# Kernel tuning notes

Hardware: AMD Instinct MI355X
Metric: run time of the kernel (lower is better)

Reference implementation:

```python
import jax, jax.numpy as jnp
import numpy as np
from jax import lax

B, T, PRED_LEN = 1024, 100, 30
E, H, IN = 512, 1024, 2


def _gru_cell(h, gx, Whh, bhh):
    # PyTorch GRU cell. gx = x @ Wih.T + bih precomputed, shape (B, 3H).
    gh = h @ Whh.T + bhh
    gx_r, gx_z, gx_n = jnp.split(gx, 3, axis=-1)
    gh_r, gh_z, gh_n = jnp.split(gh, 3, axis=-1)
    r = jax.nn.sigmoid(gx_r + gh_r)
    z = jax.nn.sigmoid(gx_z + gh_z)
    n = jnp.tanh(gx_n + r * gh_n)
    return (1.0 - z) * n + z * h


def _run_gru(x, h0, Wih, Whh, bih, bhh):
    # x: (B, T, F) -> outputs (B, T, H), final hidden (B, H)
    gx = jnp.einsum('btf,gf->btg', x, Wih) + bih  # batch all input projections
    def step(h, gxt):
        h_new = _gru_cell(h, gxt, Whh, bhh)
        return h_new, h_new
    h_last, ys = lax.scan(step, h0, jnp.swapaxes(gx, 0, 1))
    return jnp.swapaxes(ys, 0, 1), h_last


def setup_inputs() -> dict:
    key = jax.random.key(0)
    ks = iter(jax.random.split(key, 32))
    s = 1.0 / np.sqrt(H)
    u = lambda k, shp: jax.random.uniform(k, shp, jnp.float32, -s, s)
    inp = {'obs': jax.random.normal(next(ks), (B, T, IN), jnp.float32)}
    inp['We'] = u(next(ks), (E, IN)); inp['be'] = u(next(ks), (E,))
    inp['Wed'] = u(next(ks), (E, 2)); inp['bed'] = u(next(ks), (E,))
    for name, fin in [('enc1', E), ('enc2', H), ('dec1', E), ('dec2', H)]:
        inp[name + '_Wih'] = u(next(ks), (3 * H, fin))
        inp[name + '_Whh'] = u(next(ks), (3 * H, H))
        inp[name + '_bih'] = u(next(ks), (3 * H,))
        inp[name + '_bhh'] = u(next(ks), (3 * H,))
    inp['Wout'] = u(next(ks), (2, H)); inp['bout'] = u(next(ks), (2,))
    return inp


def reference(obs, We, be, Wed, bed,
              enc1_Wih, enc1_Whh, enc1_bih, enc1_bhh,
              enc2_Wih, enc2_Whh, enc2_bih, enc2_bhh,
              dec1_Wih, dec1_Whh, dec1_bih, dec1_bhh,
              dec2_Wih, dec2_Whh, dec2_bih, dec2_bhh,
              Wout, bout):
    b = obs.shape[0]
    h0 = jnp.zeros((b, H), obs.dtype)
    # --- encoder ---
    emb = jnp.tanh(jnp.einsum('bti,ei->bte', obs, We) + be)
    enc1, h = _run_gru(emb, h0, enc1_Wih, enc1_Whh, enc1_bih, enc1_bhh)
    # quirk preserved: hidden from gru1 is fed as h0 of gru2
    enc2, h = _run_gru(enc1, h, enc2_Wih, enc2_Whh, enc2_bih, enc2_bhh)
    out_loc0 = enc2[:, -2, :] @ Wout.T + bout  # second-to-last step (B, 2)
    def dec_step(carry, _):
        hc, last = carry
        d_emb = jnp.tanh(last @ Wed.T + bed)
        h1 = _gru_cell(hc, d_emb @ dec1_Wih.T + dec1_bih, dec1_Whh, dec1_bhh)
        h2 = _gru_cell(h1, h1 @ dec2_Wih.T + dec2_bih, dec2_Whh, dec2_bhh)
        out = h2 @ Wout.T + bout
        return (h2, out), out
    _, preds = lax.scan(dec_step, (h, out_loc0), None, length=PRED_LEN)
    return jnp.swapaxes(preds, 0, 1)  # (B, pred_len, 2)
```

## Files before the change

### kernel.cpp

```cpp
#include <hip/hip_runtime.h>
#include <stdint.h>

#define NB 1024
#define NT 100
#define NPRED 30
#define NE 512
#define NH 1024
#define NG (3*NH)

typedef unsigned short u16;
typedef unsigned int u32;
typedef u16 u16x4 __attribute__((ext_vector_type(4)));
typedef float f32x4 __attribute__((ext_vector_type(4)));
typedef __bf16 bf16x8 __attribute__((ext_vector_type(8)));

__device__ __forceinline__ u16 f2b(float f){
  u32 u = __float_as_uint(f);
  u = (u + 0x7FFFu + ((u >> 16) & 1u)) >> 16;
  return (u16)u;
}
__device__ __forceinline__ float sig_(float x){ return 1.0f/(1.0f+__expf(-x)); }
__device__ __forceinline__ float tanh_(float x){
  float e = __expf(2.0f*fabsf(x));
  return copysignf(1.0f - 2.0f/(e+1.0f), x);
}

__global__ void cvt_kernel(const float* src, u16* dst, int n4){
  int i = blockIdx.x*256 + threadIdx.x;
  if (i < n4){
    f32x4 v = ((const f32x4*)src)[i];
    u16x4 o;
    o[0]=f2b(v[0]); o[1]=f2b(v[1]); o[2]=f2b(v[2]); o[3]=f2b(v[3]);
    ((u16x4*)dst)[i] = o;
  }
}

__global__ void emb_kernel(const float* __restrict__ obs, const float* __restrict__ We,
                           const float* __restrict__ be, u16* __restrict__ out, int t){
  int idx = blockIdx.x*256 + threadIdx.x;
  int b = idx >> 9, e = idx & 511;
  float x0 = obs[(b*NT + t)*2], x1 = obs[(b*NT + t)*2 + 1];
  out[idx] = f2b(tanh_(We[e*2]*x0 + We[e*2+1]*x1 + be[e]));
}

__device__ __forceinline__ void gload16(const u16* g, const u16* lds){
  __builtin_amdgcn_global_load_lds(
      (const __attribute__((address_space(1))) void*)g,
      (__attribute__((address_space(3))) void*)lds, 16, 0, 0);
}

__device__ __forceinline__ void gemm_tile_body(
    const u16* __restrict__ A, int lda,
    const u16* __restrict__ W, int K,
    const float* __restrict__ bias, float* __restrict__ C,
    int bRow, int bCol)
{
  __shared__ __align__(16) u16 As[2][128][64];
  __shared__ __align__(16) u16 Bs[2][128][64];

  const int tid = threadIdx.x;
  const int w = tid >> 6, l = tid & 63;
  const int wm = w >> 1, wn = w & 1;
  const int fr = l & 15, lhi = l >> 4;
  const int srow = l >> 3;
  const int gcol = (((l & 7) ^ srow) * 8);

  f32x4 acc[4][4];
  #pragma unroll
  for (int m=0;m<4;m++)
    #pragma unroll
    for (int n=0;n<4;n++) acc[m][n] = (f32x4)0.0f;

  const u16* Ab = A + (size_t)bRow*lda + gcol;
  const u16* Wb = W + (size_t)bCol*K + gcol;
  const int NK = K >> 6;

  #pragma unroll
  for (int s4=0;s4<4;s4++){
    int slab = w*4 + s4;
    int row = slab*8 + srow;
    gload16(Ab + (size_t)row*lda, &As[0][slab*8][0]);
    gload16(Wb + (size_t)row*K,   &Bs[0][slab*8][0]);
  }
  __syncthreads();

  for (int t = 0; t < NK; ++t){
    const int cur = t & 1;
    if (t + 1 < NK){
      const int k0 = (t+1)*64;
      #pragma unroll
      for (int s4=0;s4<4;s4++){
        int slab = w*4 + s4;
        int row = slab*8 + srow;
        gload16(Ab + (size_t)row*lda + k0, &As[cur^1][slab*8][0]);
        gload16(Wb + (size_t)row*K   + k0, &Bs[cur^1][slab*8][0]);
      }
    }
    const u16* Ac = &As[cur][0][0];
    const u16* Bc = &Bs[cur][0][0];
    #pragma unroll
    for (int kk=0; kk<2; ++kk){
      const int ch = (((kk*4 + lhi) ^ (l & 7)) * 8);
      bf16x8 af[4], bfr[4];
      #pragma unroll
      for (int m=0;m<4;m++)
        af[m] = *(const bf16x8*)(Ac + (size_t)(wm*64 + m*16 + fr)*64 + ch);
      #pragma unroll
      for (int n=0;n<4;n++)
        bfr[n] = *(const bf16x8*)(Bc + (size_t)(wn*64 + n*16 + fr)*64 + ch);
      #pragma unroll
      for (int m=0;m<4;m++)
        #pragma unroll
        for (int n=0;n<4;n++)
          acc[m][n] = __builtin_amdgcn_mfma_f32_16x16x32_bf16(af[m], bfr[n], acc[m][n], 0, 0, 0);
    }
    __syncthreads();
  }

  const int crow = lhi * 4, ccol = l & 15;
  #pragma unroll
  for (int n=0;n<4;n++){
    int col = bCol + wn*64 + n*16 + ccol;
    float bv = bias[col];
    #pragma unroll
    for (int m=0;m<4;m++){
      int row = bRow + wm*64 + m*16 + crow;
      float* Cp = C + (size_t)row*NG + col;
      #pragma unroll
      for (int r=0;r<4;r++)
        __builtin_nontemporal_store(acc[m][n][r] + bv, Cp + (size_t)r*NG);
    }
  }
}

__global__ __launch_bounds__(256)
void gemm_dual_kernel(
  const u16* A0, int lda0, int K0, const u16* W0, const float* bias0, float* C0,
  const u16* A1, int lda1, int K1, const u16* W1, const float* bias1, float* C1)
{
  const int id = blockIdx.x;
  const int xcd = id & 7, k = id >> 3;
  const int cb = 3*xcd + (k >> 4);
  const int rem = k & 15;
  const int rb = rem >> 1;
  const int z  = rem & 1;

  if (z == 0)
    gemm_tile_body(A0, lda0, W0, K0, bias0, C0, rb*128, cb*128);
  else
    gemm_tile_body(A1, lda1, W1, K1, bias1, C1, rb*128, cb*128);
}

__device__ __forceinline__ void cell_core(
    const float* __restrict__ gx, const float* __restrict__ gh,
    const float* __restrict__ hin, float* __restrict__ hout,
    u16* __restrict__ houtb, u16* __restrict__ seq,
    int b, int jq, f32x4& o)
{
  int idx = b*256 + jq;
  int base = b*768;
  const f32x4* gx4 = (const f32x4*)gx;
  const f32x4* gh4 = (const f32x4*)gh;
  f32x4 xr = gx4[base + jq], xz = gx4[base + 256 + jq], xn = gx4[base + 512 + jq];
  f32x4 hr = gh4[base + jq], hz = gh4[base + 256 + jq], hn = gh4[base + 512 + jq];
  f32x4 hv = ((const f32x4*)hin)[idx];
  u16x4 ob;
  #pragma unroll
  for (int c=0;c<4;c++){
    float r = sig_(xr[c] + hr[c]);
    float z = sig_(xz[c] + hz[c]);
    float n = tanh_(xn[c] + r*hn[c]);
    float h = (1.0f - z)*n + z*hv[c];
    o[c] = h; ob[c] = f2b(h);
  }
  ((f32x4*)hout)[idx] = o;
  ((u16x4*)houtb)[idx] = ob;
  if (seq) ((u16x4*)seq)[idx] = ob;
}

__global__ void gru_cell_kernel(const float* __restrict__ gx, const float* __restrict__ gh,
                                const float* __restrict__ hin, float* __restrict__ hout,
                                u16* __restrict__ houtb, u16* __restrict__ seq)
{
  f32x4 o;
  cell_core(gx, gh, hin, hout, houtb, seq, blockIdx.x, threadIdx.x, o);
}

__global__ void gru_cell_emb_kernel(const float* __restrict__ gx, const float* __restrict__ gh,
                                    const float* __restrict__ hin, float* __restrict__ hout,
                                    u16* __restrict__ houtb, u16* __restrict__ seq,
                                    const float* __restrict__ obs, const float* __restrict__ We,
                                    const float* __restrict__ be, u16* __restrict__ embb, int et)
{
  int b = blockIdx.x, tid = threadIdx.x;
  f32x4 o;
  cell_core(gx, gh, hin, hout, houtb, seq, b, tid, o);
  if (embb){
    float x0 = obs[(b*NT + et)*2], x1 = obs[(b*NT + et)*2 + 1];
    int e0 = tid*2;
    u16 v0 = f2b(tanh_(We[e0*2]  *x0 + We[e0*2+1]*x1 + be[e0]));
    u16 v1 = f2b(tanh_(We[e0*2+2]*x0 + We[e0*2+3]*x1 + be[e0+1]));
    ((u32*)embb)[b*256 + tid] = (u32)v0 | ((u32)v1 << 16);
  }
}

__global__ void gru_cell_out_kernel(const float* __restrict__ gx, const float* __restrict__ gh,
                                    const float* __restrict__ hin, float* __restrict__ hout,
                                    u16* __restrict__ houtb,
                                    const float* __restrict__ Wout, const float* __restrict__ bout,
                                    float* __restrict__ dout, int ot,
                                    const float* __restrict__ Wed, const float* __restrict__ bed,
                                    u16* __restrict__ dembb)
{
  int b = blockIdx.x, tid = threadIdx.x;
  f32x4 o;
  cell_core(gx, gh, hin, hout, houtb, (u16*)nullptr, b, tid, o);

  int j0 = tid*4;
  float s0 = 0.f, s1 = 0.f;
  #pragma unroll
  for (int c=0;c<4;c++){
    s0 += o[c]*Wout[j0+c];
    s1 += o[c]*Wout[NH + j0 + c];
  }
  #pragma unroll
  for (int off = 32; off > 0; off >>= 1){
    s0 += __shfl_down(s0, off);
    s1 += __shfl_down(s1, off);
  }
  __shared__ float red[8];
  __shared__ float lastsh[2];
  int w = tid >> 6;
  if ((tid & 63) == 0){ red[w*2] = s0; red[w*2+1] = s1; }
  __syncthreads();
  if (tid == 0){
    float o0 = red[0]+red[2]+red[4]+red[6] + bout[0];
    float o1 = red[1]+red[3]+red[5]+red[7] + bout[1];
    lastsh[0] = o0; lastsh[1] = o1;
    if (dout){ dout[(size_t)b*(NPRED*2) + ot*2]     = o0;
               dout[(size_t)b*(NPRED*2) + ot*2 + 1] = o1; }
  }
  __syncthreads();
  float x0 = lastsh[0], x1 = lastsh[1];
  int e0 = tid*2;
  u16 v0 = f2b(tanh_(Wed[e0*2]  *x0 + Wed[e0*2+1]*x1 + bed[e0]));
  u16 v1 = f2b(tanh_(Wed[e0*2+2]*x0 + Wed[e0*2+3]*x1 + bed[e0+1]));
  ((u32*)dembb)[b*256 + tid] = (u32)v0 | ((u32)v1 << 16);
}

extern "C" void kernel_launch(void* const* d_in, const int* in_sizes, int n_in,
                              void* d_out, int out_size, void* d_ws, size_t ws_size,
                              hipStream_t stream)
{
  (void)in_sizes; (void)n_in; (void)out_size;
  const float* obs  = (const float*)d_in[0];
  const float* We   = (const float*)d_in[1];
  const float* be   = (const float*)d_in[2];
  const float* Wed  = (const float*)d_in[3];
  const float* bed  = (const float*)d_in[4];
  const float* e1Wih = (const float*)d_in[5];
  const float* e1Whh = (const float*)d_in[6];
  const float* e1bih = (const float*)d_in[7];
  const float* e1bhh = (const float*)d_in[8];
  const float* e2Wih = (const float*)d_in[9];
  const float* e2Whh = (const float*)d_in[10];
  const float* e2bih = (const float*)d_in[11];
  const float* e2bhh = (const float*)d_in[12];
  const float* d1Wih = (const float*)d_in[13];
  const float* d1Whh = (const float*)d_in[14];
  const float* d1bih = (const float*)d_in[15];
  const float* d1bhh = (const float*)d_in[16];
  const float* d2Wih = (const float*)d_in[17];
  const float* d2Whh = (const float*)d_in[18];
  const float* d2bih = (const float*)d_in[19];
  const float* d2bhh = (const float*)d_in[20];
  const float* Wout = (const float*)d_in[21];
  const float* bout = (const float*)d_in[22];
  float* out = (float*)d_out;

  char* ws = (char*)d_ws;
  size_t off = 0;
  auto alloc = [&](size_t bytes)->char* {
    char* p = ws + off;
    off += (bytes + 255) & ~(size_t)255;
    return p;
  };
  u16* wE1i = (u16*)alloc((size_t)NG*NE*2);
  u16* wE1h = (u16*)alloc((size_t)NG*NH*2);
  u16* wE2i = (u16*)alloc((size_t)NG*NH*2);
  u16* wE2h = (u16*)alloc((size_t)NG*NH*2);
  u16* wD1i = (u16*)alloc((size_t)NG*NE*2);
  u16* wD1h = (u16*)alloc((size_t)NG*NH*2);
  u16* wD2i = (u16*)alloc((size_t)NG*NH*2);
  u16* wD2h = (u16*)alloc((size_t)NG*NH*2);
  u16* embb  = (u16*)alloc((size_t)NB*NE*2);
  u16* dembb = (u16*)alloc((size_t)NB*NE*2);
  float* h1f = (float*)alloc((size_t)NB*NH*4);
  u16*   h1b = (u16*)alloc((size_t)NB*NH*2);
  float* h2f = (float*)alloc((size_t)NB*NH*4);
  u16*   h2b = (u16*)alloc((size_t)NB*NH*2);
  float* gx  = (float*)alloc((size_t)NB*NG*4);
  float* gh  = (float*)alloc((size_t)NB*NG*4);

  const size_t slot = (size_t)NB*NH*2;
  size_t avail = (ws_size > off + (1u<<20)) ? (ws_size - off - (1u<<20)) : 0;
  int cs = (int)(avail / slot);
  if (cs > NT) cs = NT;
  u16* cache = (u16*)alloc((size_t)cs * slot);
  const int cache_start = NT - cs;

  hipMemsetAsync(h1f, 0, (size_t)NB*NH*4, stream);
  hipMemsetAsync(h1b, 0, (size_t)NB*NH*2, stream);

  auto cvt = [&](const float* src, u16* dst, size_t n){
    int n4 = (int)(n >> 2);
    cvt_kernel<<<dim3((n4 + 255)/256), dim3(256), 0, stream>>>(src, dst, n4);
  };
  cvt(e1Wih, wE1i, (size_t)NG*NE);
  cvt(e1Whh, wE1h, (size_t)NG*NH);
  cvt(e2Wih, wE2i, (size_t)NG*NH);
  cvt(e2Whh, wE2h, (size_t)NG*NH);
  cvt(d1Wih, wD1i, (size_t)NG*NE);
  cvt(d1Whh, wD1h, (size_t)NG*NH);
  cvt(d2Wih, wD2i, (size_t)NG*NH);
  cvt(d2Whh, wD2h, (size_t)NG*NH);

  const dim3 blk(256);
  const dim3 dual_grid(384);
  const dim3 emb_grid((NB*NE)/256);
  const dim3 cell_grid(NB);

  emb_kernel<<<emb_grid, blk, 0, stream>>>(obs, We, be, embb, 0);
  for (int t = 0; t < NT; ++t){
    gemm_dual_kernel<<<dual_grid, blk, 0, stream>>>(
        embb, NE, NE, wE1i, e1bih, gx,
        h1b,  NH, NH, wE1h, e1bhh, gh);
    u16* slot_p = (t >= cache_start) ? cache + (size_t)(t - cache_start)*NB*NH : (u16*)nullptr;
    gru_cell_emb_kernel<<<cell_grid, blk, 0, stream>>>(
        gx, gh, h1f, h1f, h1b, slot_p,
        obs, We, be, (t+1 < NT) ? embb : (u16*)nullptr, t+1);
  }

  hipMemcpyAsync(h2f, h1f, (size_t)NB*NH*4, hipMemcpyDeviceToDevice, stream);
  hipMemcpyAsync(h2b, h1b, (size_t)NB*NH*2, hipMemcpyDeviceToDevice, stream);

  if (cache_start > 0){
    hipMemsetAsync(h1f, 0, (size_t)NB*NH*4, stream);
    hipMemsetAsync(h1b, 0, (size_t)NB*NH*2, stream);
    emb_kernel<<<emb_grid, blk, 0, stream>>>(obs, We, be, embb, 0);
  }
  for (int t = 0; t < cache_start; ++t){
    gemm_dual_kernel<<<dual_grid, blk, 0, stream>>>(
        embb, NE, NE, wE1i, e1bih, gx,
        h1b,  NH, NH, wE1h, e1bhh, gh);
    gru_cell_emb_kernel<<<cell_grid, blk, 0, stream>>>(
        gx, gh, h1f, h1f, h1b, (u16*)nullptr,
        obs, We, be, (t+1 < cache_start) ? embb : (u16*)nullptr, t+1);
    gemm_dual_kernel<<<dual_grid, blk, 0, stream>>>(
        h1b, NH, NH, wE2i, e2bih, gx,
        h2b, NH, NH, wE2h, e2bhh, gh);
    if (t == NT - 2)
      gru_cell_out_kernel<<<cell_grid, blk, 0, stream>>>(
          gx, gh, h2f, h2f, h2b, Wout, bout, (float*)nullptr, 0, Wed, bed, dembb);
    else
      gru_cell_kernel<<<cell_grid, blk, 0, stream>>>(gx, gh, h2f, h2f, h2b, (u16*)nullptr);
  }
  for (int t = cache_start; t < NT; ++t){
    const u16* enc1_t = cache + (size_t)(t - cache_start)*NB*NH;
    gemm_dual_kernel<<<dual_grid, blk, 0, stream>>>(
        enc1_t, NH, NH, wE2i, e2bih, gx,
        h2b,    NH, NH, wE2h, e2bhh, gh);
    if (t == NT - 2)
      gru_cell_out_kernel<<<cell_grid, blk, 0, stream>>>(
          gx, gh, h2f, h2f, h2b, Wout, bout, (float*)nullptr, 0, Wed, bed, dembb);
    else
      gru_cell_kernel<<<cell_grid, blk, 0, stream>>>(gx, gh, h2f, h2f, h2b, (u16*)nullptr);
  }

  for (int t = 0; t < NPRED; ++t){
    gemm_dual_kernel<<<dual_grid, blk, 0, stream>>>(
        dembb, NE, NE, wD1i, d1bih, gx,
        h2b,   NH, NH, wD1h, d1bhh, gh);
    gru_cell_kernel<<<cell_grid, blk, 0, stream>>>(gx, gh, h2f, h1f, h1b, (u16*)nullptr);
    gemm_dual_kernel<<<dual_grid, blk, 0, stream>>>(
        h1b, NH, NH, wD2i, d2bih, gx,
        h1b, NH, NH, wD2h, d2bhh, gh);
    gru_cell_out_kernel<<<cell_grid, blk, 0, stream>>>(
        gx, gh, h1f, h2f, h2b, Wout, bout, out, t, Wed, bed, dembb);
  }
}
```

Measured before the change: 8.224 ms.

## Fuse GRU cell update into dual GEMM via last-arriving-block counters

Merges the GRU cell elementwise kernel into the gate GEMM kernel. Each block bumps an atomic counter for its (row-block, hidden-slice) group, and the sixth block to arrive (three gates times the gx and gh halves) computes the cell update for that 128x128 hidden tile, including the next-step embedding. Hidden-state bf16 buffers and embedding buffers are double-buffered so that blocks still reading the previous state are not overwritten. This removes one launch and one full pass over gx/gh per step, at the cost of atomics, threadfences, and imbalance on the tail block. It also drops the nontemporal stores so the freshly written gates can stay in cache.

```diff
diff --git a/kernel.cpp b/kernel.cpp
--- a/kernel.cpp
+++ b/kernel.cpp
@@ -53,11 +53,9 @@
     const u16* __restrict__ A, int lda,
     const u16* __restrict__ W, int K,
     const float* __restrict__ bias, float* __restrict__ C,
-    int bRow, int bCol)
+    int bRow, int bCol,
+    u16 (*As)[128][64], u16 (*Bs)[128][64])
 {
-  __shared__ __align__(16) u16 As[2][128][64];
-  __shared__ __align__(16) u16 Bs[2][128][64];
-
   const int tid = threadIdx.x;
   const int w = tid >> 6, l = tid & 63;
   const int wm = w >> 1, wn = w & 1;
@@ -127,17 +125,24 @@
       int row = bRow + wm*64 + m*16 + crow;
       float* Cp = C + (size_t)row*NG + col;
       #pragma unroll
-      for (int r=0;r<4;r++)
-        __builtin_nontemporal_store(acc[m][n][r] + bv, Cp + (size_t)r*NG);
+      for (int r=0;r<4;r++) Cp[(size_t)r*NG] = acc[m][n][r] + bv;
     }
   }
 }
 
 __global__ __launch_bounds__(256)
-void gemm_dual_kernel(
+void gemm_dual_cell_kernel(
   const u16* A0, int lda0, int K0, const u16* W0, const float* bias0, float* C0,
-  const u16* A1, int lda1, int K1, const u16* W1, const float* bias1, float* C1)
+  const u16* A1, int lda1, int K1, const u16* W1, const float* bias1, float* C1,
+  u32* __restrict__ counters,
+  const float* __restrict__ hin, float* __restrict__ houtf,
+  u16* __restrict__ houtb, u16* __restrict__ seq,
+  const float* __restrict__ obs, const float* __restrict__ We,
+  const float* __restrict__ be, u16* __restrict__ embb, int et)
 {
+  __shared__ __align__(16) u16 As[2][128][64];
+  __shared__ __align__(16) u16 Bs[2][128][64];
+
   const int id = blockIdx.x;
   const int xcd = id & 7, k = id >> 3;
   const int cb = 3*xcd + (k >> 4);
@@ -146,61 +151,63 @@
   const int z  = rem & 1;
 
   if (z == 0)
-    gemm_tile_body(A0, lda0, W0, K0, bias0, C0, rb*128, cb*128);
+    gemm_tile_body(A0, lda0, W0, K0, bias0, C0, rb*128, cb*128, As, Bs);
   else
-    gemm_tile_body(A1, lda1, W1, K1, bias1, C1, rb*128, cb*128);
-}
-
-__device__ __forceinline__ void cell_core(
-    const float* __restrict__ gx, const float* __restrict__ gh,
-    const float* __restrict__ hin, float* __restrict__ hout,
-    u16* __restrict__ houtb, u16* __restrict__ seq,
-    int b, int jq, f32x4& o)
-{
-  int idx = b*256 + jq;
-  int base = b*768;
-  const f32x4* gx4 = (const f32x4*)gx;
-  const f32x4* gh4 = (const f32x4*)gh;
-  f32x4 xr = gx4[base + jq], xz = gx4[base + 256 + jq], xn = gx4[base + 512 + jq];
-  f32x4 hr = gh4[base + jq], hz = gh4[base + 256 + jq], hn = gh4[base + 512 + jq];
-  f32x4 hv = ((const f32x4*)hin)[idx];
-  u16x4 ob;
-  #pragma unroll
-  for (int c=0;c<4;c++){
-    float r = sig_(xr[c] + hr[c]);
-    float z = sig_(xz[c] + hz[c]);
-    float n = tanh_(xn[c] + r*hn[c]);
-    float h = (1.0f - z)*n + z*hv[c];
-    o[c] = h; ob[c] = f2b(h);
-  }
-  ((f32x4*)hout)[idx] = o;
-  ((u16x4*)houtb)[idx] = ob;
-  if (seq) ((u16x4*)seq)[idx] = ob;
-}
-
-__global__ void gru_cell_kernel(const float* __restrict__ gx, const float* __restrict__ gh,
-                                const float* __restrict__ hin, float* __restrict__ hout,
-                                u16* __restrict__ houtb, u16* __restrict__ seq)
-{
-  f32x4 o;
-  cell_core(gx, gh, hin, hout, houtb, seq, blockIdx.x, threadIdx.x, o);
-}
-
-__global__ void gru_cell_emb_kernel(const float* __restrict__ gx, const float* __restrict__ gh,
-                                    const float* __restrict__ hin, float* __restrict__ hout,
-                                    u16* __restrict__ houtb, u16* __restrict__ seq,
-                                    const float* __restrict__ obs, const float* __restrict__ We,
-                                    const float* __restrict__ be, u16* __restrict__ embb, int et)
-{
-  int b = blockIdx.x, tid = threadIdx.x;
-  f32x4 o;
-  cell_core(gx, gh, hin, hout, houtb, seq, b, tid, o);
-  if (embb){
-    float x0 = obs[(b*NT + et)*2], x1 = obs[(b*NT + et)*2 + 1];
-    int e0 = tid*2;
-    u16 v0 = f2b(tanh_(We[e0*2]  *x0 + We[e0*2+1]*x1 + be[e0]));
-    u16 v1 = f2b(tanh_(We[e0*2+2]*x0 + We[e0*2+3]*x1 + be[e0+1]));
-    ((u32*)embb)[b*256 + tid] = (u32)v0 | ((u32)v1 << 16);
+    gemm_tile_body(A1, lda1, W1, K1, bias1, C1, rb*128, cb*128, As, Bs);
+
+  if (!counters) return;
+
+  const int tid = threadIdx.x;
+  __threadfence();
+  __syncthreads();
+  volatile u32* flag = (volatile u32*)&As[0][0][0];
+  if (tid == 0)
+    *flag = atomicAdd(&counters[rb*8 + (cb & 7)], 1u);
+  __syncthreads();
+  if (*flag != 5) return;
+  __threadfence();
+
+  const int hb = cb & 7;
+  const int row0 = rb * 128;
+  const f32x4* gx4 = (const f32x4*)C0;
+  const f32x4* gh4 = (const f32x4*)C1;
+  const f32x4* hin4 = (const f32x4*)hin;
+
+  for (int it = 0; it < 16; ++it){
+    int q = it*256 + tid;
+    int r = q >> 5, cq = q & 31;
+    int row = row0 + r;
+    size_t gb = (size_t)row*768 + hb*32 + cq;
+    f32x4 xr = gx4[gb], xz = gx4[gb + 256], xn = gx4[gb + 512];
+    f32x4 hr = gh4[gb], hz = gh4[gb + 256], hn = gh4[gb + 512];
+    size_t hq = (size_t)row*256 + hb*32 + cq;
+    f32x4 hv = hin4[hq];
+    f32x4 o; u16x4 ob;
+    #pragma unroll
+    for (int c=0;c<4;c++){
+      float rr = sig_(xr[c] + hr[c]);
+      float zz = sig_(xz[c] + hz[c]);
+      float nn = tanh_(xn[c] + rr*hn[c]);
+      float h = (1.0f - zz)*nn + zz*hv[c];
+      o[c] = h; ob[c] = f2b(h);
+    }
+    ((f32x4*)houtf)[hq] = o;
+    ((u16x4*)houtb)[hq] = ob;
+    if (seq) ((u16x4*)seq)[hq] = ob;
+  }
+
+  if (embb && hb < 4){
+    for (int it = 0; it < 32; ++it){
+      int q = it*256 + tid;
+      int r = q >> 6, cu = q & 63;
+      int row = row0 + r;
+      float x0 = obs[((size_t)row*NT + et)*2];
+      float x1 = obs[((size_t)row*NT + et)*2 + 1];
+      int e0 = hb*128 + cu*2;
+      u16 v0 = f2b(tanh_(We[e0*2]  *x0 + We[e0*2+1]*x1 + be[e0]));
+      u16 v1 = f2b(tanh_(We[e0*2+2]*x0 + We[e0*2+3]*x1 + be[e0+1]));
+      ((u32*)embb)[(size_t)row*256 + hb*64 + cu] = (u32)v0 | ((u32)v1 << 16);
+    }
   }
 }
 
@@ -213,8 +220,24 @@
                                     u16* __restrict__ dembb)
 {
   int b = blockIdx.x, tid = threadIdx.x;
-  f32x4 o;
-  cell_core(gx, gh, hin, hout, houtb, (u16*)nullptr, b, tid, o);
+  int idx = b*256 + tid;
+  int base = b*768;
+  const f32x4* gx4 = (const f32x4*)gx;
+  const f32x4* gh4 = (const f32x4*)gh;
+  f32x4 xr = gx4[base + tid], xz = gx4[base + 256 + tid], xn = gx4[base + 512 + tid];
+  f32x4 hr = gh4[base + tid], hz = gh4[base + 256 + tid], hn = gh4[base + 512 + tid];
+  f32x4 hv = ((const f32x4*)hin)[idx];
+  f32x4 o; u16x4 ob;
+  #pragma unroll
+  for (int c=0;c<4;c++){
+    float r = sig_(xr[c] + hr[c]);
+    float z = sig_(xz[c] + hz[c]);
+    float n = tanh_(xn[c] + r*hn[c]);
+    float h = (1.0f - z)*n + z*hv[c];
+    o[c] = h; ob[c] = f2b(h);
+  }
+  ((f32x4*)hout)[idx] = o;
+  ((u16x4*)houtb)[idx] = ob;
 
   int j0 = tid*4;
   float s0 = 0.f, s1 = 0.f;
@@ -293,14 +316,15 @@
   u16* wD1h = (u16*)alloc((size_t)NG*NH*2);
   u16* wD2i = (u16*)alloc((size_t)NG*NH*2);
   u16* wD2h = (u16*)alloc((size_t)NG*NH*2);
-  u16* embb  = (u16*)alloc((size_t)NB*NE*2);
+  u16* embbP[2] = { (u16*)alloc((size_t)NB*NE*2), (u16*)alloc((size_t)NB*NE*2) };
   u16* dembb = (u16*)alloc((size_t)NB*NE*2);
   float* h1f = (float*)alloc((size_t)NB*NH*4);
-  u16*   h1b = (u16*)alloc((size_t)NB*NH*2);
+  u16*   h1bP[2] = { (u16*)alloc((size_t)NB*NH*2), (u16*)alloc((size_t)NB*NH*2) };
   float* h2f = (float*)alloc((size_t)NB*NH*4);
-  u16*   h2b = (u16*)alloc((size_t)NB*NH*2);
+  u16*   h2bP[2] = { (u16*)alloc((size_t)NB*NH*2), (u16*)alloc((size_t)NB*NH*2) };
   float* gx  = (float*)alloc((size_t)NB*NG*4);
   float* gh  = (float*)alloc((size_t)NB*NG*4);
+  u32* counters = (u32*)alloc(336*64*4);
 
   const size_t slot = (size_t)NB*NH*2;
   size_t avail = (ws_size > off + (1u<<20)) ? (ws_size - off - (1u<<20)) : 0;
@@ -310,7 +334,10 @@
   const int cache_start = NT - cs;
 
   hipMemsetAsync(h1f, 0, (size_t)NB*NH*4, stream);
-  hipMemsetAsync(h1b, 0, (size_t)NB*NH*2, stream);
+  hipMemsetAsync(h1bP[0], 0, (size_t)NB*NH*2, stream);
+  hipMemsetAsync(counters, 0, 336*64*4, stream);
+  int cstep = 0;
+  auto ctr = [&]()->u32* { return counters + (cstep++)*64; };
 
   auto cvt = [&](const float* src, u16* dst, size_t n){
     int n4 = (int)(n >> 2);
@@ -328,64 +355,88 @@
   const dim3 blk(256);
   const dim3 dual_grid(384);
   const dim3 emb_grid((NB*NE)/256);
-  const dim3 cell_grid(NB);
-
-  emb_kernel<<<emb_grid, blk, 0, stream>>>(obs, We, be, embb, 0);
+
+  int p1 = 0, p2 = 0, pe = 0;
+
+  emb_kernel<<<emb_grid, blk, 0, stream>>>(obs, We, be, embbP[0], 0);
   for (int t = 0; t < NT; ++t){
-    gemm_dual_kernel<<<dual_grid, blk, 0, stream>>>(
-        embb, NE, NE, wE1i, e1bih, gx,
-        h1b,  NH, NH, wE1h, e1bhh, gh);
     u16* slot_p = (t >= cache_start) ? cache + (size_t)(t - cache_start)*NB*NH : (u16*)nullptr;
-    gru_cell_emb_kernel<<<cell_grid, blk, 0, stream>>>(
-        gx, gh, h1f, h1f, h1b, slot_p,
-        obs, We, be, (t+1 < NT) ? embb : (u16*)nullptr, t+1);
+    u16* embn = (t + 1 < NT) ? embbP[pe^1] : (u16*)nullptr;
+    gemm_dual_cell_kernel<<<dual_grid, blk, 0, stream>>>(
+        embbP[pe], NE, NE, wE1i, e1bih, gx,
+        h1bP[p1],  NH, NH, wE1h, e1bhh, gh,
+        ctr(), h1f, h1f, h1bP[p1^1], slot_p,
+        obs, We, be, embn, t+1);
+    p1 ^= 1; pe ^= 1;
   }
 
   hipMemcpyAsync(h2f, h1f, (size_t)NB*NH*4, hipMemcpyDeviceToDevice, stream);
-  hipMemcpyAsync(h2b, h1b, (size_t)NB*NH*2, hipMemcpyDeviceToDevice, stream);
+  hipMemcpyAsync(h2bP[0], h1bP[p1], (size_t)NB*NH*2, hipMemcpyDeviceToDevice, stream);
+  p2 = 0;
 
   if (cache_start > 0){
     hipMemsetAsync(h1f, 0, (size_t)NB*NH*4, stream);
-    hipMemsetAsync(h1b, 0, (size_t)NB*NH*2, stream);
-    emb_kernel<<<emb_grid, blk, 0, stream>>>(obs, We, be, embb, 0);
+    hipMemsetAsync(h1bP[0], 0, (size_t)NB*NH*2, stream);
+    p1 = 0; pe = 0;
+    emb_kernel<<<emb_grid, blk, 0, stream>>>(obs, We, be, embbP[0], 0);
   }
   for (int t = 0; t < cache_start; ++t){
-    gemm_dual_kernel<<<dual_grid, blk, 0, stream>>>(
-        embb, NE, NE, wE1i, e1bih, gx,
-        h1b,  NH, NH, wE1h, e1bhh, gh);
-    gru_cell_emb_kernel<<<cell_grid, blk, 0, stream>>>(
-        gx, gh, h1f, h1f, h1b, (u16*)nullptr,
-        obs, We, be, (t+1 < cache_start) ? embb : (u16*)nullptr, t+1);
-    gemm_dual_kernel<<<dual_grid, blk, 0, stream>>>(
-        h1b, NH, NH, wE2i, e2bih, gx,
-        h2b, NH, NH, wE2h, e2bhh, gh);
-    if (t == NT - 2)
-      gru_cell_out_kernel<<<cell_grid, blk, 0, stream>>>(
-          gx, gh, h2f, h2f, h2b, Wout, bout, (float*)nullptr, 0, Wed, bed, dembb);
-    else
-      gru_cell_kernel<<<cell_grid, blk, 0, stream>>>(gx, gh, h2f, h2f, h2b, (u16*)nullptr);
+    u16* embn = (t + 1 < cache_start) ? embbP[pe^1] : (u16*)nullptr;
+    gemm_dual_cell_kernel<<<dual_grid, blk, 0, stream>>>(
+        embbP[pe], NE, NE, wE1i, e1bih, gx,
+        h1bP[p1],  NH, NH, wE1h, e1bhh, gh,
+        ctr(), h1f, h1f, h1bP[p1^1], (u16*)nullptr,
+        obs, We, be, embn, t+1);
+    p1 ^= 1; pe ^= 1;
+    if (t == NT - 2){
+      gemm_dual_cell_kernel<<<dual_grid, blk, 0, stream>>>(
+          h1bP[p1], NH, NH, wE2i, e2bih, gx,
+          h2bP[p2], NH, NH, wE2h, e2bhh, gh,
+          (u32*)nullptr, nullptr, nullptr, nullptr, nullptr,
+          nullptr, nullptr, nullptr, nullptr, 0);
+      gru_cell_out_kernel<<<dim3(NB), blk, 0, stream>>>(
+          gx, gh, h2f, h2f, h2bP[p2^1], Wout, bout, (float*)nullptr, 0, Wed, bed, dembb);
+    } else {
+      gemm_dual_cell_kernel<<<dual_grid, blk, 0, stream>>>(
+          h1bP[p1], NH, NH, wE2i, e2bih, gx,
+          h2bP[p2], NH, NH, wE2h, e2bhh, gh,
+          ctr(), h2f, h2f, h2bP[p2^1], (u16*)nullptr,
+          nullptr, nullptr, nullptr, nullptr, 0);
+    }
+    p2 ^= 1;
   }
   for (int t = cache_start; t < NT; ++t){
     const u16* enc1_t = cache + (size_t)(t - cache_start)*NB*NH;
-    gemm_dual_kernel<<<dual_grid, blk, 0, stream>>>(
-        enc1_t, NH, NH, wE2i, e2bih, gx,
-        h2b,    NH, NH, wE2h, e2bhh, gh);
-    if (t == NT - 2)
-      gru_cell_out_kernel<<<cell_grid, blk, 0, stream>>>(
-          gx, gh, h2f, h2f, h2b, Wout, bout, (float*)nullptr, 0, Wed, bed, dembb);
-    else
-      gru_cell_kernel<<<cell_grid, blk, 0, stream>>>(gx, gh, h2f, h2f, h2b, (u16*)nullptr);
+    if (t == NT - 2){
+      gemm_dual_cell_kernel<<<dual_grid, blk, 0, stream>>>(
+          enc1_t,   NH, NH, wE2i, e2bih, gx,
+          h2bP[p2], NH, NH, wE2h, e2bhh, gh,
+          (u32*)nullptr, nullptr, nullptr, nullptr, nullptr,
+          nullptr, nullptr, nullptr, nullptr, 0);
+      gru_cell_out_kernel<<<dim3(NB), blk, 0, stream>>>(
+          gx, gh, h2f, h2f, h2bP[p2^1], Wout, bout, (float*)nullptr, 0, Wed, bed, dembb);
+    } else {
+      gemm_dual_cell_kernel<<<dual_grid, blk, 0, stream>>>(
+          enc1_t,   NH, NH, wE2i, e2bih, gx,
+          h2bP[p2], NH, NH, wE2h, e2bhh, gh,
+          ctr(), h2f, h2f, h2bP[p2^1], (u16*)nullptr,
+          nullptr, nullptr, nullptr, nullptr, 0);
+    }
+    p2 ^= 1;
   }
 
   for (int t = 0; t < NPRED; ++t){
-    gemm_dual_kernel<<<dual_grid, blk, 0, stream>>>(
-        dembb, NE, NE, wD1i, d1bih, gx,
-        h2b,   NH, NH, wD1h, d1bhh, gh);
-    gru_cell_kernel<<<cell_grid, blk, 0, stream>>>(gx, gh, h2f, h1f, h1b, (u16*)nullptr);
-    gemm_dual_kernel<<<dual_grid, blk, 0, stream>>>(
-        h1b, NH, NH, wD2i, d2bih, gx,
-        h1b, NH, NH, wD2h, d2bhh, gh);
-    gru_cell_out_kernel<<<cell_grid, blk, 0, stream>>>(
-        gx, gh, h1f, h2f, h2b, Wout, bout, out, t, Wed, bed, dembb);
-  }
-}
+    gemm_dual_cell_kernel<<<dual_grid, blk, 0, stream>>>(
+        dembb,    NE, NE, wD1i, d1bih, gx,
+        h2bP[p2], NH, NH, wD1h, d1bhh, gh,
+        ctr(), h2f, h1f, h1bP[0], (u16*)nullptr,
+        nullptr, nullptr, nullptr, nullptr, 0);
+    gemm_dual_cell_kernel<<<dual_grid, blk, 0, stream>>>(
+        h1bP[0], NH, NH, wD2i, d2bih, gx,
+        h1bP[0], NH, NH, wD2h, d2bhh, gh,
+        (u32*)nullptr, nullptr, nullptr, nullptr, nullptr,
+        nullptr, nullptr, nullptr, nullptr, 0);
+    gru_cell_out_kernel<<<dim3(NB), blk, 0, stream>>>(
+        gx, gh, h1f, h2f, h2bP[p2], Wout, bout, out, t, Wed, bed, dembb);
+  }
+}
```

Measured after the change: 24.78 ms. 201% more time.

## Load GEMM A fragments directly into registers instead of staging through LDS

Applied to the files above, without the earlier changes.

The A operand of the batched input-projection GEMM tile is now read straight from global memory into per-wave register fragments, with one k-tile prefetched ahead. Only the weight tile still goes through double-buffered LDS. This halves LDS footprint and LDS read traffic, but each wave pair now loads the same A rows redundantly from global/L2 with less-coalesced 16-byte loads. Register pressure also rises from holding two sets of A fragments.

```diff
diff --git a/kernel.cpp b/kernel.cpp
--- a/kernel.cpp
+++ b/kernel.cpp
@@ -55,7 +55,6 @@
     const float* __restrict__ bias, float* __restrict__ C,
     int bRow, int bCol)
 {
-  __shared__ __align__(16) u16 As[2][128][64];
   __shared__ __align__(16) u16 Bs[2][128][64];
 
   const int tid = threadIdx.x;
@@ -71,51 +70,61 @@
     #pragma unroll
     for (int n=0;n<4;n++) acc[m][n] = (f32x4)0.0f;
 
-  const u16* Ab = A + (size_t)bRow*lda + gcol;
+  const u16* Afrag = A + (size_t)(bRow + wm*64 + fr)*lda + lhi*8;
   const u16* Wb = W + (size_t)bCol*K + gcol;
   const int NK = K >> 6;
 
-  #pragma unroll
-  for (int s4=0;s4<4;s4++){
-    int slab = w*4 + s4;
-    int row = slab*8 + srow;
-    gload16(Ab + (size_t)row*lda, &As[0][slab*8][0]);
-    gload16(Wb + (size_t)row*K,   &Bs[0][slab*8][0]);
-  }
+  bf16x8 aA[8], aB[8];
+
+  #define PREF_A(ar, kt) do { \
+    const u16* _ap = Afrag + (size_t)(kt)*64; \
+    _Pragma("unroll") \
+    for (int m=0;m<4;m++){ \
+      ar[m]     = *(const bf16x8*)(_ap + (size_t)m*16*lda); \
+      ar[4 + m] = *(const bf16x8*)(_ap + (size_t)m*16*lda + 32); \
+    } } while(0)
+
+  #define STAGE_W(buf, kt) do { int _k0 = (kt)*64; \
+    _Pragma("unroll") \
+    for (int s4=0;s4<4;s4++){ \
+      int slab = w*4 + s4; \
+      int row = slab*8 + srow; \
+      gload16(Wb + (size_t)row*K + _k0, &Bs[(buf)][slab*8][0]); \
+    } } while(0)
+
+  #define COMP(buf, ar) do { \
+    _Pragma("unroll") \
+    for (int kk=0; kk<2; ++kk){ \
+      const int ch = (((kk*4 + lhi) ^ (l & 7)) * 8); \
+      bf16x8 bfr[4]; \
+      _Pragma("unroll") \
+      for (int n=0;n<4;n++) \
+        bfr[n] = *(const bf16x8*)(&Bs[(buf)][wn*64 + n*16 + fr][0] + ch); \
+      _Pragma("unroll") \
+      for (int m=0;m<4;m++) \
+        _Pragma("unroll") \
+        for (int n=0;n<4;n++) \
+          acc[m][n] = __builtin_amdgcn_mfma_f32_16x16x32_bf16(ar[kk*4 + m], bfr[n], acc[m][n], 0, 0, 0); \
+    } } while(0)
+
+  PREF_A(aA, 0);
+  STAGE_W(0, 0);
   __syncthreads();
 
-  for (int t = 0; t < NK; ++t){
-    const int cur = t & 1;
-    if (t + 1 < NK){
-      const int k0 = (t+1)*64;
-      #pragma unroll
-      for (int s4=0;s4<4;s4++){
-        int slab = w*4 + s4;
-        int row = slab*8 + srow;
-        gload16(Ab + (size_t)row*lda + k0, &As[cur^1][slab*8][0]);
-        gload16(Wb + (size_t)row*K   + k0, &Bs[cur^1][slab*8][0]);
-      }
-    }
-    const u16* Ac = &As[cur][0][0];
-    const u16* Bc = &Bs[cur][0][0];
-    #pragma unroll
-    for (int kk=0; kk<2; ++kk){
-      const int ch = (((kk*4 + lhi) ^ (l & 7)) * 8);
-      bf16x8 af[4], bfr[4];
-      #pragma unroll
-      for (int m=0;m<4;m++)
-        af[m] = *(const bf16x8*)(Ac + (size_t)(wm*64 + m*16 + fr)*64 + ch);
-      #pragma unroll
-      for (int n=0;n<4;n++)
-        bfr[n] = *(const bf16x8*)(Bc + (size_t)(wn*64 + n*16 + fr)*64 + ch);
-      #pragma unroll
-      for (int m=0;m<4;m++)
-        #pragma unroll
-        for (int n=0;n<4;n++)
-          acc[m][n] = __builtin_amdgcn_mfma_f32_16x16x32_bf16(af[m], bfr[n], acc[m][n], 0, 0, 0);
-    }
+  for (int t = 0; t < NK; t += 2){
+    if (t + 1 < NK) STAGE_W(1, t + 1);
+    PREF_A(aB, (t + 1 < NK) ? t + 1 : 0);
+    COMP(0, aA);
     __syncthreads();
-  }
+    if (t + 2 < NK) STAGE_W(0, t + 2);
+    PREF_A(aA, (t + 2 < NK) ? t + 2 : 0);
+    COMP(1, aB);
+    __syncthreads();
+  }
+
+  #undef PREF_A
+  #undef STAGE_W
+  #undef COMP
 
   const int crow = lhi * 4, ccol = l & 15;
   #pragma unroll
```

Measured after the change: 13.01 ms. +58.1%, slower.
